# Optimization experiments

Measured on AMD Instinct MI355X. Metric: run time of the kernel, lower is better.

The kernel has to match this reference:

```python
import jax, jax.numpy as jnp
import numpy as np

H = 1024   # hidden_size
I = 2048   # intermediate_size
E = 16     # num_experts
K = 2      # num_experts_per_tok
B, T = 2, 2048


def setup_inputs() -> dict:
    key = jax.random.key(0)
    k1, k2, k3, k4 = jax.random.split(key, 4)
    x = jax.random.normal(k1, (B, T, H), dtype=jnp.float32)
    # torch nn.Linear weight layout: [out_features, in_features]
    Wg = jax.random.normal(k2, (E, H), dtype=jnp.float32) * 0.02   # gate
    W1 = jax.random.normal(k3, (E, I, H), dtype=jnp.float32) * 0.02  # fc1 per expert
    W2 = jax.random.normal(k4, (E, H, I), dtype=jnp.float32) * 0.02  # fc2 per expert
    return {"x": x, "Wg": Wg, "W1": W1, "W2": W2}


def reference(x, Wg, W1, W2):
    Bq, Tq, Hq = x.shape
    nt = Bq * Tq
    x_flat = x.reshape(nt, Hq)                       # [nt, H]
    gate_logits = x_flat @ Wg.T                      # [nt, E]
    gate_probs = jax.nn.softmax(gate_logits, axis=-1)
    topk_vals, topk_idx = jax.lax.top_k(gate_probs, K)  # [nt, K]
    # dense combine weights: zero for unselected (token, expert) pairs
    rows = jnp.arange(nt)[:, None]                   # [nt, 1]
    cw = jnp.zeros((nt, E), dtype=x.dtype).at[rows, topk_idx].add(topk_vals)
    # per-expert dense SiLU-MLP; combine weight of 0 makes unselected
    # contributions exactly zero, matching the original gather/scatter math.
    y_flat = jnp.zeros_like(x_flat)
    for e in range(E):
        h = jax.nn.silu(x_flat @ W1[e].T)            # [nt, I]
        o = h @ W2[e].T                              # [nt, H]
        y_flat = y_flat + cw[:, e:e + 1] * o
    return y_flat.reshape(Bq, Tq, Hq)
```

## Files before the change

kernel.cpp:

```cpp
#include <hip/hip_runtime.h>
#include <hip/hip_bf16.h>

#define H_DIM 1024
#define I_DIM 2048
#define NEXP  16
#define NTOK  4096
#define BM 128
#define BN 128
#define BK 32
#define ABUF (BM*BK)
#define BBUF (BN*BK)
#define MAXS 10240
#define MAXRB (MAXS/BM)
#define PAIRS (NTOK*2)
#define SORT_T 256
#define PPT (PAIRS/SORT_T)

typedef __attribute__((ext_vector_type(8))) short short8;
typedef __attribute__((ext_vector_type(4))) short short4v;
typedef __attribute__((ext_vector_type(4))) float f32x4;

#define OFF_TOKE 256
#define OFF_TOKW (OFF_TOKE + PAIRS*4)
#define OFF_TOS  (OFF_TOKW + PAIRS*4)
#define OFF_WOS  (OFF_TOS + MAXS*4)
#define OFF_H    (OFF_WOS + MAXS*4)
#define OFF_XBF  (OFF_H + (size_t)MAXS*I_DIM*2)
#define OFF_WBF  (OFF_XBF + (size_t)NTOK*H_DIM*2)
#define NEED_FULL (OFF_WBF + (size_t)NEXP*I_DIM*H_DIM*2)

#define GLDS16(gsrc, ldst) \
  __builtin_amdgcn_global_load_lds((const __attribute__((address_space(1))) void*)(gsrc), \
                                   (__attribute__((address_space(3))) void*)(ldst), 16, 0, 0)

__device__ inline short f2bf(float f) {
    union { float f; unsigned u; } v; v.f = f;
    unsigned u = v.u + 0x7FFFu + ((v.u >> 16) & 1u);
    return (short)(u >> 16);
}

__device__ inline short8 pack8(const float4 a, const float4 b) {
    return (short8){ f2bf(a.x), f2bf(a.y), f2bf(a.z), f2bf(a.w),
                     f2bf(b.x), f2bf(b.y), f2bf(b.z), f2bf(b.w) };
}

__global__ __launch_bounds__(256) void conv_kernel(
    const float* __restrict__ src, short* __restrict__ dst, int n8)
{
    int i = blockIdx.x * blockDim.x + threadIdx.x;
    const int stride = gridDim.x * blockDim.x;
    for (; i < n8; i += stride) {
        const float4 f0 = ((const float4*)src)[2*i];
        const float4 f1 = ((const float4*)src)[2*i+1];
        ((short8*)dst)[i] = pack8(f0, f1);
    }
}

template<bool WRITE_XBF>
__global__ __launch_bounds__(256) void gate_kernel(
    const float* __restrict__ x, const float* __restrict__ Wg,
    int* __restrict__ tokE, float* __restrict__ tokW, short* __restrict__ xbf)
{
    const int tok  = blockIdx.x * 4 + (threadIdx.x >> 6);
    const int lane = threadIdx.x & 63;
    const float4* xr = (const float4*)(x + (size_t)tok * H_DIM);

    float acc[NEXP];
#pragma unroll
    for (int e = 0; e < NEXP; e++) acc[e] = 0.f;
#pragma unroll
    for (int j = 0; j < H_DIM/4; j += 64) {
        const float4 xv = xr[j + lane];
        if constexpr (WRITE_XBF) {
            *(short4v*)(xbf + (size_t)tok * H_DIM + (j + lane) * 4) =
                (short4v){ f2bf(xv.x), f2bf(xv.y), f2bf(xv.z), f2bf(xv.w) };
        }
#pragma unroll
        for (int e = 0; e < NEXP; e++) {
            const float4 wv = ((const float4*)(Wg + e * H_DIM))[j + lane];
            acc[e] = fmaf(xv.x, wv.x, fmaf(xv.y, wv.y, fmaf(xv.z, wv.z, fmaf(xv.w, wv.w, acc[e]))));
        }
    }
#pragma unroll
    for (int off = 32; off; off >>= 1) {
#pragma unroll
        for (int e = 0; e < NEXP; e++) acc[e] += __shfl_xor(acc[e], off, 64);
    }
    if (lane == 0) {
        float m = acc[0];
#pragma unroll
        for (int e = 1; e < NEXP; e++) m = fmaxf(m, acc[e]);
        float p[NEXP]; float s = 0.f;
#pragma unroll
        for (int e = 0; e < NEXP; e++) { p[e] = __expf(acc[e] - m); s += p[e]; }
        int i1 = 0;
#pragma unroll
        for (int e = 1; e < NEXP; e++) if (acc[e] > acc[i1]) i1 = e;
        int i2 = -1;
#pragma unroll
        for (int e = 0; e < NEXP; e++) {
            if (e == i1) continue;
            if (i2 < 0 || acc[e] > acc[i2]) i2 = e;
        }
        const float inv = 1.f / s;
        tokE[tok*2+0] = i1; tokW[tok*2+0] = p[i1] * inv;
        tokE[tok*2+1] = i2; tokW[tok*2+1] = p[i2] * inv;
    }
}

__global__ __launch_bounds__(SORT_T) void sort_kernel(
    const int* __restrict__ tokE, const float* __restrict__ tokW,
    int* __restrict__ aoff, int* __restrict__ tok_of_slot, float* __restrict__ w_of_slot)
{
    __shared__ int hist[NEXP * SORT_T];
    __shared__ int tot[NEXP];
    __shared__ int aoff_l[NEXP + 1];

    const int tid = threadIdx.x;
    const int lane = tid & 63, wv = tid >> 6;

    int eloc[PPT];
#pragma unroll
    for (int i = 0; i < PPT; i++) eloc[i] = tokE[tid * PPT + i];

#pragma unroll
    for (int e = 0; e < NEXP; e++) hist[e * SORT_T + tid] = 0;
    __syncthreads();
#pragma unroll
    for (int i = 0; i < PPT; i++) hist[eloc[i] * SORT_T + tid]++;
    __syncthreads();

#pragma unroll
    for (int r = 0; r < 4; r++) {
        const int e = wv * 4 + r;
        const int base = e * SORT_T + lane * 4;
        int v0 = hist[base+0], v1 = hist[base+1], v2 = hist[base+2], v3 = hist[base+3];
        const int s = v0 + v1 + v2 + v3;
        int incl = s;
#pragma unroll
        for (int off = 1; off < 64; off <<= 1) {
            const int t = __shfl_up(incl, off, 64);
            if (lane >= off) incl += t;
        }
        int run = incl - s;
        hist[base+0] = run; run += v0;
        hist[base+1] = run; run += v1;
        hist[base+2] = run; run += v2;
        hist[base+3] = run;
        if (lane == 63) tot[e] = incl;
    }
    __syncthreads();

    if (tid == 0) {
        int acc = 0;
#pragma unroll
        for (int e = 0; e < NEXP; e++) {
            aoff_l[e] = acc; aoff[e] = acc;
            acc += ((tot[e] + BM - 1) / BM) * BM;
        }
        aoff_l[NEXP] = acc; aoff[NEXP] = acc;
    }
    __syncthreads();

#pragma unroll
    for (int i = 0; i < PPT; i++) {
        const int p = tid * PPT + i;
        const int e = eloc[i];
        const int idx = hist[e * SORT_T + tid]++;
        const int slot = aoff_l[e] + idx;
        tok_of_slot[slot] = p >> 1;
        w_of_slot[slot] = tokW[p];
    }
}

template<int MODE>
__global__ __launch_bounds__(256) void fc1_kernel_t(
    const void* __restrict__ xsrc, const void* __restrict__ w1src,
    const int* __restrict__ aoff, const int* __restrict__ tok_of_slot,
    short* __restrict__ h)
{
    const int total = aoff[NEXP];
    const int row0 = blockIdx.y * BM;
    if (row0 >= total) return;
    int e = 0;
    while (aoff[e+1] <= row0) e++;
    const int col0 = blockIdx.x * BN;

    __shared__ short As[2*ABUF];
    __shared__ short Bs[2*BBUF];

    const int tid = threadIdx.x, wid = tid>>6, lane = tid&63;
    const int wr = wid>>1, wc = wid&1;

    const int srow = wid*32 + (lane>>2);
    const int skc  = (lane&3)*8;

    int t0 = tok_of_slot[row0 + srow];      if (t0 < 0) t0 = 0;
    int t1 = tok_of_slot[row0 + srow + 16]; if (t1 < 0) t1 = 0;

    const short *sa0=nullptr,*sa1=nullptr,*sb0=nullptr,*sb1=nullptr;
    const float *fa0=nullptr,*fa1=nullptr,*fb0=nullptr,*fb1=nullptr;
    if constexpr (MODE == 0) {
        const short* xb = (const short*)xsrc;
        const short* wb = (const short*)w1src + (size_t)e * I_DIM * H_DIM;
        sa0 = xb + (size_t)t0 * H_DIM + skc;
        sa1 = xb + (size_t)t1 * H_DIM + skc;
        sb0 = wb + (size_t)(col0 + srow)      * H_DIM + skc;
        sb1 = wb + (size_t)(col0 + srow + 16) * H_DIM + skc;
    } else {
        const float* xf = (const float*)xsrc;
        const float* wf = (const float*)w1src + (size_t)e * I_DIM * H_DIM;
        fa0 = xf + (size_t)t0 * H_DIM + skc;
        fa1 = xf + (size_t)t1 * H_DIM + skc;
        fb0 = wf + (size_t)(col0 + srow)      * H_DIM + skc;
        fb1 = wf + (size_t)(col0 + srow + 16) * H_DIM + skc;
    }
    short* la0 = &As[(wid*2+0)*512];
    short* la1 = &As[(wid*2+1)*512];
    short* lb0 = &Bs[(wid*2+0)*512];
    short* lb1 = &Bs[(wid*2+1)*512];

    const int frow = lane & 15, fko = (lane>>4)*8;

    f32x4 acc[4][4];
#pragma unroll
    for (int m=0;m<4;m++)
#pragma unroll
        for (int n=0;n<4;n++) acc[m][n] = (f32x4){0.f,0.f,0.f,0.f};

#define FC1_STAGE(buf, k)                                                     \
    if constexpr (MODE == 0) {                                                \
        GLDS16(sa0 + (k), la0 + (buf)*ABUF);                                  \
        GLDS16(sa1 + (k), la1 + (buf)*ABUF);                                  \
        GLDS16(sb0 + (k), lb0 + (buf)*BBUF);                                  \
        GLDS16(sb1 + (k), lb1 + (buf)*BBUF);                                  \
    } else {                                                                  \
        const float4 a00 = *(const float4*)(fa0+(k)), a01 = *(const float4*)(fa0+(k)+4); \
        const float4 a10 = *(const float4*)(fa1+(k)), a11 = *(const float4*)(fa1+(k)+4); \
        const float4 b00 = *(const float4*)(fb0+(k)), b01 = *(const float4*)(fb0+(k)+4); \
        const float4 b10 = *(const float4*)(fb1+(k)), b11 = *(const float4*)(fb1+(k)+4); \
        *(short8*)&As[(buf)*ABUF + srow*32 + skc]      = pack8(a00, a01);     \
        *(short8*)&As[(buf)*ABUF + (srow+16)*32 + skc] = pack8(a10, a11);     \
        *(short8*)&Bs[(buf)*BBUF + srow*32 + skc]      = pack8(b00, b01);     \
        *(short8*)&Bs[(buf)*BBUF + (srow+16)*32 + skc] = pack8(b10, b11);     \
    }

    FC1_STAGE(0, 0);
    __syncthreads();

    const int NT = H_DIM / BK;
    int cur = 0;
    for (int t = 0; t < NT; ++t) {
        if (t + 1 < NT) { FC1_STAGE(cur ^ 1, (t + 1) * BK); }

        short8 af[4], bfr[4];
#pragma unroll
        for (int m=0;m<4;m++) af[m]  = *(const short8*)&As[cur*ABUF + (wr*64 + m*16 + frow)*32 + fko];
#pragma unroll
        for (int n=0;n<4;n++) bfr[n] = *(const short8*)&Bs[cur*BBUF + (wc*64 + n*16 + frow)*32 + fko];
#pragma unroll
        for (int m=0;m<4;m++)
#pragma unroll
            for (int n=0;n<4;n++)
                acc[m][n] = __builtin_amdgcn_mfma_f32_16x16x32_bf16(af[m], bfr[n], acc[m][n], 0, 0, 0);

        __syncthreads();
        cur ^= 1;
    }
#undef FC1_STAGE

    const int mr0 = row0 + wr*64 + (lane>>4)*4;
    const int nc0 = col0 + wc*64 + (lane&15);
#pragma unroll
    for (int m=0;m<4;m++)
#pragma unroll
        for (int n=0;n<4;n++)
#pragma unroll
            for (int r=0;r<4;r++) {
                const float v = acc[m][n][r];
                const float sv = v / (1.f + __expf(-v));
                h[(size_t)(mr0 + m*16 + r) * I_DIM + nc0 + n*16] = f2bf(sv);
            }
}

template<int MODE>
__global__ __launch_bounds__(256) void fc2_kernel_t(
    const short* __restrict__ h, const void* __restrict__ w2src,
    const int* __restrict__ aoff, const int* __restrict__ tok_of_slot,
    const float* __restrict__ w_of_slot, float* __restrict__ y)
{
    const int total = aoff[NEXP];
    const int row0 = blockIdx.y * BM;
    if (row0 >= total) return;
    int e = 0;
    while (aoff[e+1] <= row0) e++;
    const int col0 = blockIdx.x * BN;

    __shared__ short As[2*ABUF];
    __shared__ short Bs[2*BBUF];

    const int tid = threadIdx.x, wid = tid>>6, lane = tid&63;
    const int wr = wid>>1, wc = wid&1;

    const int srow = wid*32 + (lane>>2);
    const int skc  = (lane&3)*8;

    const short* sa0 = h + (size_t)(row0 + srow)      * I_DIM + skc;
    const short* sa1 = h + (size_t)(row0 + srow + 16) * I_DIM + skc;

    const short *sb0=nullptr,*sb1=nullptr;
    const float *fb0=nullptr,*fb1=nullptr;
    if constexpr (MODE == 0) {
        const short* wb = (const short*)w2src + (size_t)e * H_DIM * I_DIM;
        sb0 = wb + (size_t)(col0 + srow)      * I_DIM + skc;
        sb1 = wb + (size_t)(col0 + srow + 16) * I_DIM + skc;
    } else {
        const float* wf = (const float*)w2src + (size_t)e * H_DIM * I_DIM;
        fb0 = wf + (size_t)(col0 + srow)      * I_DIM + skc;
        fb1 = wf + (size_t)(col0 + srow + 16) * I_DIM + skc;
    }
    short* la0 = &As[(wid*2+0)*512];
    short* la1 = &As[(wid*2+1)*512];
    short* lb0 = &Bs[(wid*2+0)*512];
    short* lb1 = &Bs[(wid*2+1)*512];

    const int frow = lane & 15, fko = (lane>>4)*8;

    f32x4 acc[4][4];
#pragma unroll
    for (int m=0;m<4;m++)
#pragma unroll
        for (int n=0;n<4;n++) acc[m][n] = (f32x4){0.f,0.f,0.f,0.f};

#define FC2_STAGE(buf, k)                                                     \
    {                                                                         \
        GLDS16(sa0 + (k), la0 + (buf)*ABUF);                                  \
        GLDS16(sa1 + (k), la1 + (buf)*ABUF);                                  \
        if constexpr (MODE == 0) {                                            \
            GLDS16(sb0 + (k), lb0 + (buf)*BBUF);                              \
            GLDS16(sb1 + (k), lb1 + (buf)*BBUF);                              \
        } else {                                                              \
            const float4 b00 = *(const float4*)(fb0+(k)), b01 = *(const float4*)(fb0+(k)+4); \
            const float4 b10 = *(const float4*)(fb1+(k)), b11 = *(const float4*)(fb1+(k)+4); \
            *(short8*)&Bs[(buf)*BBUF + srow*32 + skc]      = pack8(b00, b01); \
            *(short8*)&Bs[(buf)*BBUF + (srow+16)*32 + skc] = pack8(b10, b11); \
        }                                                                     \
    }

    FC2_STAGE(0, 0);
    __syncthreads();

    const int NT = I_DIM / BK;
    int cur = 0;
    for (int t = 0; t < NT; ++t) {
        if (t + 1 < NT) { FC2_STAGE(cur ^ 1, (t + 1) * BK); }

        short8 af[4], bfr[4];
#pragma unroll
        for (int m=0;m<4;m++) af[m]  = *(const short8*)&As[cur*ABUF + (wr*64 + m*16 + frow)*32 + fko];
#pragma unroll
        for (int n=0;n<4;n++) bfr[n] = *(const short8*)&Bs[cur*BBUF + (wc*64 + n*16 + frow)*32 + fko];
#pragma unroll
        for (int m=0;m<4;m++)
#pragma unroll
            for (int n=0;n<4;n++)
                acc[m][n] = __builtin_amdgcn_mfma_f32_16x16x32_bf16(af[m], bfr[n], acc[m][n], 0, 0, 0);

        __syncthreads();
        cur ^= 1;
    }
#undef FC2_STAGE

    const int mr0 = row0 + wr*64 + (lane>>4)*4;
    const int nc0 = col0 + wc*64 + (lane&15);
#pragma unroll
    for (int m=0;m<4;m++)
#pragma unroll
        for (int r=0;r<4;r++) {
            const int slot = mr0 + m*16 + r;
            const int tok = tok_of_slot[slot];
            if (tok < 0) continue;
            const float w = w_of_slot[slot];
#pragma unroll
            for (int n=0;n<4;n++)
                atomicAdd(&y[(size_t)tok * H_DIM + nc0 + n*16], w * acc[m][n][r]);
        }
}

extern "C" void kernel_launch(void* const* d_in, const int* in_sizes, int n_in,
                              void* d_out, int out_size, void* d_ws, size_t ws_size,
                              hipStream_t stream) {
    const float* x  = (const float*)d_in[0];
    const float* Wg = (const float*)d_in[1];
    const float* W1 = (const float*)d_in[2];
    const float* W2 = (const float*)d_in[3];
    float* y = (float*)d_out;

    char* ws = (char*)d_ws;
    int*   aoff        = (int*)  (ws + 128);
    int*   tokE        = (int*)  (ws + OFF_TOKE);
    float* tokW        = (float*)(ws + OFF_TOKW);
    int*   tok_of_slot = (int*)  (ws + OFF_TOS);
    float* w_of_slot   = (float*)(ws + OFF_WOS);
    short* h           = (short*)(ws + OFF_H);
    short* xbf         = (short*)(ws + OFF_XBF);
    short* wbf         = (short*)(ws + OFF_WBF);

    const bool full = (ws_size >= NEED_FULL);

    hipMemsetAsync(tok_of_slot, 0xFF, MAXS*4, stream);
    hipMemsetAsync(y, 0, (size_t)out_size * 4, stream);

    if (full) {
        gate_kernel<true><<<NTOK/4, 256, 0, stream>>>(x, Wg, tokE, tokW, xbf);
        sort_kernel<<<1, SORT_T, 0, stream>>>(tokE, tokW, aoff, tok_of_slot, w_of_slot);
        conv_kernel<<<2048, 256, 0, stream>>>(W1, wbf, NEXP*I_DIM*H_DIM/8);
        fc1_kernel_t<0><<<dim3(I_DIM/BN, MAXRB), 256, 0, stream>>>(xbf, wbf, aoff, tok_of_slot, h);
        conv_kernel<<<2048, 256, 0, stream>>>(W2, wbf, NEXP*H_DIM*I_DIM/8);
        fc2_kernel_t<0><<<dim3(H_DIM/BN, MAXRB), 256, 0, stream>>>(h, wbf, aoff, tok_of_slot, w_of_slot, y);
    } else {
        gate_kernel<false><<<NTOK/4, 256, 0, stream>>>(x, Wg, tokE, tokW, nullptr);
        sort_kernel<<<1, SORT_T, 0, stream>>>(tokE, tokW, aoff, tok_of_slot, w_of_slot);
        fc1_kernel_t<1><<<dim3(I_DIM/BN, MAXRB), 256, 0, stream>>>(x, W1, aoff, tok_of_slot, h);
        fc2_kernel_t<1><<<dim3(H_DIM/BN, MAXRB), 256, 0, stream>>>(h, W2, aoff, tok_of_slot, w_of_slot, y);
    }
}
```

Before: 278.0 us.

## Convert fp32 expert weights to bf16 inside GEMM loads, drop pre-conversion passes

Removes the two standalone kernels that converted all of W1 and W2 to bf16 in workspace. The fc1/fc2 kernels now read fp32 weights directly into registers, issue those loads before the MFMA block and write them to LDS as bf16 afterwards, so load latency is hidden behind compute. It also flattens the grid to 1D with an XCD-aware block swizzle to improve L2 locality. This avoids writing and re-reading about 128MB of converted weights, at the cost of doubled weight bytes per tile read and extra VALU packing inside the main loop.

```diff
diff --git a/kernel.cpp b/kernel.cpp
--- a/kernel.cpp
+++ b/kernel.cpp
@@ -12,6 +12,8 @@
 #define BBUF (BN*BK)
 #define MAXS 10240
 #define MAXRB (MAXS/BM)
+#define NC1 (I_DIM/BN)
+#define NC2 (H_DIM/BN)
 #define PAIRS (NTOK*2)
 #define SORT_T 256
 #define PPT (PAIRS/SORT_T)
@@ -26,8 +28,7 @@
 #define OFF_WOS  (OFF_TOS + MAXS*4)
 #define OFF_H    (OFF_WOS + MAXS*4)
 #define OFF_XBF  (OFF_H + (size_t)MAXS*I_DIM*2)
-#define OFF_WBF  (OFF_XBF + (size_t)NTOK*H_DIM*2)
-#define NEED_FULL (OFF_WBF + (size_t)NEXP*I_DIM*H_DIM*2)
+#define NEED_XBF (OFF_XBF + (size_t)NTOK*H_DIM*2)
 
 #define GLDS16(gsrc, ldst) \
   __builtin_amdgcn_global_load_lds((const __attribute__((address_space(1))) void*)(gsrc), \
@@ -44,16 +45,8 @@
                      f2bf(b.x), f2bf(b.y), f2bf(b.z), f2bf(b.w) };
 }
 
-__global__ __launch_bounds__(256) void conv_kernel(
-    const float* __restrict__ src, short* __restrict__ dst, int n8)
-{
-    int i = blockIdx.x * blockDim.x + threadIdx.x;
-    const int stride = gridDim.x * blockDim.x;
-    for (; i < n8; i += stride) {
-        const float4 f0 = ((const float4*)src)[2*i];
-        const float4 f1 = ((const float4*)src)[2*i+1];
-        ((short8*)dst)[i] = pack8(f0, f1);
-    }
+__device__ inline int xcd_swz(int bid, int nwg) {
+    return (bid & 7) * (nwg >> 3) + (bid >> 3);
 }
 
 template<bool WRITE_XBF>
@@ -173,52 +166,48 @@
     }
 }
 
-template<int MODE>
+template<int AMODE>
 __global__ __launch_bounds__(256) void fc1_kernel_t(
-    const void* __restrict__ xsrc, const void* __restrict__ w1src,
+    const void* __restrict__ xsrc, const float* __restrict__ W1,
     const int* __restrict__ aoff, const int* __restrict__ tok_of_slot,
     short* __restrict__ h)
 {
+    const int wg = xcd_swz(blockIdx.x, NC1 * MAXRB);
+    const int colb = wg % NC1, rowb = wg / NC1;
     const int total = aoff[NEXP];
-    const int row0 = blockIdx.y * BM;
+    const int row0 = rowb * BM;
     if (row0 >= total) return;
     int e = 0;
     while (aoff[e+1] <= row0) e++;
-    const int col0 = blockIdx.x * BN;
+    const int col0 = colb * BN;
 
     __shared__ short As[2*ABUF];
     __shared__ short Bs[2*BBUF];
 
     const int tid = threadIdx.x, wid = tid>>6, lane = tid&63;
     const int wr = wid>>1, wc = wid&1;
-
     const int srow = wid*32 + (lane>>2);
     const int skc  = (lane&3)*8;
 
     int t0 = tok_of_slot[row0 + srow];      if (t0 < 0) t0 = 0;
     int t1 = tok_of_slot[row0 + srow + 16]; if (t1 < 0) t1 = 0;
 
-    const short *sa0=nullptr,*sa1=nullptr,*sb0=nullptr,*sb1=nullptr;
-    const float *fa0=nullptr,*fa1=nullptr,*fb0=nullptr,*fb1=nullptr;
-    if constexpr (MODE == 0) {
+    const float* wf0 = W1 + (size_t)e * I_DIM * H_DIM + (size_t)(col0 + srow)      * H_DIM + skc;
+    const float* wf1 = W1 + (size_t)e * I_DIM * H_DIM + (size_t)(col0 + srow + 16) * H_DIM + skc;
+
+    const short *sa0=nullptr,*sa1=nullptr;
+    const float *fa0=nullptr,*fa1=nullptr;
+    if constexpr (AMODE == 0) {
         const short* xb = (const short*)xsrc;
-        const short* wb = (const short*)w1src + (size_t)e * I_DIM * H_DIM;
         sa0 = xb + (size_t)t0 * H_DIM + skc;
         sa1 = xb + (size_t)t1 * H_DIM + skc;
-        sb0 = wb + (size_t)(col0 + srow)      * H_DIM + skc;
-        sb1 = wb + (size_t)(col0 + srow + 16) * H_DIM + skc;
     } else {
         const float* xf = (const float*)xsrc;
-        const float* wf = (const float*)w1src + (size_t)e * I_DIM * H_DIM;
         fa0 = xf + (size_t)t0 * H_DIM + skc;
         fa1 = xf + (size_t)t1 * H_DIM + skc;
-        fb0 = wf + (size_t)(col0 + srow)      * H_DIM + skc;
-        fb1 = wf + (size_t)(col0 + srow + 16) * H_DIM + skc;
     }
     short* la0 = &As[(wid*2+0)*512];
     short* la1 = &As[(wid*2+1)*512];
-    short* lb0 = &Bs[(wid*2+0)*512];
-    short* lb1 = &Bs[(wid*2+1)*512];
 
     const int frow = lane & 15, fko = (lane>>4)*8;
 
@@ -228,30 +217,38 @@
 #pragma unroll
         for (int n=0;n<4;n++) acc[m][n] = (f32x4){0.f,0.f,0.f,0.f};
 
-#define FC1_STAGE(buf, k)                                                     \
-    if constexpr (MODE == 0) {                                                \
-        GLDS16(sa0 + (k), la0 + (buf)*ABUF);                                  \
-        GLDS16(sa1 + (k), la1 + (buf)*ABUF);                                  \
-        GLDS16(sb0 + (k), lb0 + (buf)*BBUF);                                  \
-        GLDS16(sb1 + (k), lb1 + (buf)*BBUF);                                  \
-    } else {                                                                  \
-        const float4 a00 = *(const float4*)(fa0+(k)), a01 = *(const float4*)(fa0+(k)+4); \
-        const float4 a10 = *(const float4*)(fa1+(k)), a11 = *(const float4*)(fa1+(k)+4); \
-        const float4 b00 = *(const float4*)(fb0+(k)), b01 = *(const float4*)(fb0+(k)+4); \
-        const float4 b10 = *(const float4*)(fb1+(k)), b11 = *(const float4*)(fb1+(k)+4); \
-        *(short8*)&As[(buf)*ABUF + srow*32 + skc]      = pack8(a00, a01);     \
-        *(short8*)&As[(buf)*ABUF + (srow+16)*32 + skc] = pack8(a10, a11);     \
-        *(short8*)&Bs[(buf)*BBUF + srow*32 + skc]      = pack8(b00, b01);     \
-        *(short8*)&Bs[(buf)*BBUF + (srow+16)*32 + skc] = pack8(b10, b11);     \
-    }
-
-    FC1_STAGE(0, 0);
+    float4 b00 = *(const float4*)(wf0), b01 = *(const float4*)(wf0+4);
+    float4 b10 = *(const float4*)(wf1), b11 = *(const float4*)(wf1+4);
+    float4 a00, a01, a10, a11;
+    if constexpr (AMODE == 0) {
+        GLDS16(sa0, la0);
+        GLDS16(sa1, la1);
+    } else {
+        a00 = *(const float4*)(fa0); a01 = *(const float4*)(fa0+4);
+        a10 = *(const float4*)(fa1); a11 = *(const float4*)(fa1+4);
+        *(short8*)&As[srow*32 + skc]      = pack8(a00, a01);
+        *(short8*)&As[(srow+16)*32 + skc] = pack8(a10, a11);
+    }
+    *(short8*)&Bs[srow*32 + skc]      = pack8(b00, b01);
+    *(short8*)&Bs[(srow+16)*32 + skc] = pack8(b10, b11);
     __syncthreads();
 
     const int NT = H_DIM / BK;
     int cur = 0;
     for (int t = 0; t < NT; ++t) {
-        if (t + 1 < NT) { FC1_STAGE(cur ^ 1, (t + 1) * BK); }
+        const int kn = (t+1)*BK;
+        const bool more = (t+1 < NT);
+        if (more) {
+            if constexpr (AMODE == 0) {
+                GLDS16(sa0 + kn, la0 + (cur^1)*ABUF);
+                GLDS16(sa1 + kn, la1 + (cur^1)*ABUF);
+            } else {
+                a00 = *(const float4*)(fa0+kn); a01 = *(const float4*)(fa0+kn+4);
+                a10 = *(const float4*)(fa1+kn); a11 = *(const float4*)(fa1+kn+4);
+            }
+            b00 = *(const float4*)(wf0+kn); b01 = *(const float4*)(wf0+kn+4);
+            b10 = *(const float4*)(wf1+kn); b11 = *(const float4*)(wf1+kn+4);
+        }
 
         short8 af[4], bfr[4];
 #pragma unroll
@@ -264,10 +261,17 @@
             for (int n=0;n<4;n++)
                 acc[m][n] = __builtin_amdgcn_mfma_f32_16x16x32_bf16(af[m], bfr[n], acc[m][n], 0, 0, 0);
 
+        if (more) {
+            if constexpr (AMODE == 1) {
+                *(short8*)&As[(cur^1)*ABUF + srow*32 + skc]      = pack8(a00, a01);
+                *(short8*)&As[(cur^1)*ABUF + (srow+16)*32 + skc] = pack8(a10, a11);
+            }
+            *(short8*)&Bs[(cur^1)*BBUF + srow*32 + skc]      = pack8(b00, b01);
+            *(short8*)&Bs[(cur^1)*BBUF + (srow+16)*32 + skc] = pack8(b10, b11);
+        }
         __syncthreads();
         cur ^= 1;
     }
-#undef FC1_STAGE
 
     const int mr0 = row0 + wr*64 + (lane>>4)*4;
     const int nc0 = col0 + wc*64 + (lane&15);
@@ -283,46 +287,36 @@
             }
 }
 
-template<int MODE>
-__global__ __launch_bounds__(256) void fc2_kernel_t(
-    const short* __restrict__ h, const void* __restrict__ w2src,
+__global__ __launch_bounds__(256) void fc2_kernel(
+    const short* __restrict__ h, const float* __restrict__ W2,
     const int* __restrict__ aoff, const int* __restrict__ tok_of_slot,
     const float* __restrict__ w_of_slot, float* __restrict__ y)
 {
+    const int wg = xcd_swz(blockIdx.x, NC2 * MAXRB);
+    const int colb = wg % NC2, rowb = wg / NC2;
     const int total = aoff[NEXP];
-    const int row0 = blockIdx.y * BM;
+    const int row0 = rowb * BM;
     if (row0 >= total) return;
     int e = 0;
     while (aoff[e+1] <= row0) e++;
-    const int col0 = blockIdx.x * BN;
+    const int col0 = colb * BN;
 
     __shared__ short As[2*ABUF];
     __shared__ short Bs[2*BBUF];
 
     const int tid = threadIdx.x, wid = tid>>6, lane = tid&63;
     const int wr = wid>>1, wc = wid&1;
-
     const int srow = wid*32 + (lane>>2);
     const int skc  = (lane&3)*8;
 
     const short* sa0 = h + (size_t)(row0 + srow)      * I_DIM + skc;
     const short* sa1 = h + (size_t)(row0 + srow + 16) * I_DIM + skc;
 
-    const short *sb0=nullptr,*sb1=nullptr;
-    const float *fb0=nullptr,*fb1=nullptr;
-    if constexpr (MODE == 0) {
-        const short* wb = (const short*)w2src + (size_t)e * H_DIM * I_DIM;
-        sb0 = wb + (size_t)(col0 + srow)      * I_DIM + skc;
-        sb1 = wb + (size_t)(col0 + srow + 16) * I_DIM + skc;
-    } else {
-        const float* wf = (const float*)w2src + (size_t)e * H_DIM * I_DIM;
-        fb0 = wf + (size_t)(col0 + srow)      * I_DIM + skc;
-        fb1 = wf + (size_t)(col0 + srow + 16) * I_DIM + skc;
-    }
+    const float* wf0 = W2 + (size_t)e * H_DIM * I_DIM + (size_t)(col0 + srow)      * I_DIM + skc;
+    const float* wf1 = W2 + (size_t)e * H_DIM * I_DIM + (size_t)(col0 + srow + 16) * I_DIM + skc;
+
     short* la0 = &As[(wid*2+0)*512];
     short* la1 = &As[(wid*2+1)*512];
-    short* lb0 = &Bs[(wid*2+0)*512];
-    short* lb1 = &Bs[(wid*2+1)*512];
 
     const int frow = lane & 15, fko = (lane>>4)*8;
 
@@ -332,28 +326,25 @@
 #pragma unroll
         for (int n=0;n<4;n++) acc[m][n] = (f32x4){0.f,0.f,0.f,0.f};
 
-#define FC2_STAGE(buf, k)                                                     \
-    {                                                                         \
-        GLDS16(sa0 + (k), la0 + (buf)*ABUF);                                  \
-        GLDS16(sa1 + (k), la1 + (buf)*ABUF);                                  \
-        if constexpr (MODE == 0) {                                            \
-            GLDS16(sb0 + (k), lb0 + (buf)*BBUF);                              \
-            GLDS16(sb1 + (k), lb1 + (buf)*BBUF);                              \
-        } else {                                                              \
-            const float4 b00 = *(const float4*)(fb0+(k)), b01 = *(const float4*)(fb0+(k)+4); \
-            const float4 b10 = *(const float4*)(fb1+(k)), b11 = *(const float4*)(fb1+(k)+4); \
-            *(short8*)&Bs[(buf)*BBUF + srow*32 + skc]      = pack8(b00, b01); \
-            *(short8*)&Bs[(buf)*BBUF + (srow+16)*32 + skc] = pack8(b10, b11); \
-        }                                                                     \
-    }
-
-    FC2_STAGE(0, 0);
+    float4 b00 = *(const float4*)(wf0), b01 = *(const float4*)(wf0+4);
+    float4 b10 = *(const float4*)(wf1), b11 = *(const float4*)(wf1+4);
+    GLDS16(sa0, la0);
+    GLDS16(sa1, la1);
+    *(short8*)&Bs[srow*32 + skc]      = pack8(b00, b01);
+    *(short8*)&Bs[(srow+16)*32 + skc] = pack8(b10, b11);
     __syncthreads();
 
     const int NT = I_DIM / BK;
     int cur = 0;
     for (int t = 0; t < NT; ++t) {
-        if (t + 1 < NT) { FC2_STAGE(cur ^ 1, (t + 1) * BK); }
+        const int kn = (t+1)*BK;
+        const bool more = (t+1 < NT);
+        if (more) {
+            GLDS16(sa0 + kn, la0 + (cur^1)*ABUF);
+            GLDS16(sa1 + kn, la1 + (cur^1)*ABUF);
+            b00 = *(const float4*)(wf0+kn); b01 = *(const float4*)(wf0+kn+4);
+            b10 = *(const float4*)(wf1+kn); b11 = *(const float4*)(wf1+kn+4);
+        }
 
         short8 af[4], bfr[4];
 #pragma unroll
@@ -366,10 +357,13 @@
             for (int n=0;n<4;n++)
                 acc[m][n] = __builtin_amdgcn_mfma_f32_16x16x32_bf16(af[m], bfr[n], acc[m][n], 0, 0, 0);
 
+        if (more) {
+            *(short8*)&Bs[(cur^1)*BBUF + srow*32 + skc]      = pack8(b00, b01);
+            *(short8*)&Bs[(cur^1)*BBUF + (srow+16)*32 + skc] = pack8(b10, b11);
+        }
         __syncthreads();
         cur ^= 1;
     }
-#undef FC2_STAGE
 
     const int mr0 = row0 + wr*64 + (lane>>4)*4;
     const int nc0 = col0 + wc*64 + (lane&15);
@@ -404,24 +398,20 @@
     float* w_of_slot   = (float*)(ws + OFF_WOS);
     short* h           = (short*)(ws + OFF_H);
     short* xbf         = (short*)(ws + OFF_XBF);
-    short* wbf         = (short*)(ws + OFF_WBF);
-
-    const bool full = (ws_size >= NEED_FULL);
+
+    const bool hasXbf = (ws_size >= NEED_XBF);
 
     hipMemsetAsync(tok_of_slot, 0xFF, MAXS*4, stream);
     hipMemsetAsync(y, 0, (size_t)out_size * 4, stream);
 
-    if (full) {
+    if (hasXbf) {
         gate_kernel<true><<<NTOK/4, 256, 0, stream>>>(x, Wg, tokE, tokW, xbf);
         sort_kernel<<<1, SORT_T, 0, stream>>>(tokE, tokW, aoff, tok_of_slot, w_of_slot);
-        conv_kernel<<<2048, 256, 0, stream>>>(W1, wbf, NEXP*I_DIM*H_DIM/8);
-        fc1_kernel_t<0><<<dim3(I_DIM/BN, MAXRB), 256, 0, stream>>>(xbf, wbf, aoff, tok_of_slot, h);
-        conv_kernel<<<2048, 256, 0, stream>>>(W2, wbf, NEXP*H_DIM*I_DIM/8);
-        fc2_kernel_t<0><<<dim3(H_DIM/BN, MAXRB), 256, 0, stream>>>(h, wbf, aoff, tok_of_slot, w_of_slot, y);
+        fc1_kernel_t<0><<<NC1*MAXRB, 256, 0, stream>>>(xbf, W1, aoff, tok_of_slot, h);
     } else {
         gate_kernel<false><<<NTOK/4, 256, 0, stream>>>(x, Wg, tokE, tokW, nullptr);
         sort_kernel<<<1, SORT_T, 0, stream>>>(tokE, tokW, aoff, tok_of_slot, w_of_slot);
-        fc1_kernel_t<1><<<dim3(I_DIM/BN, MAXRB), 256, 0, stream>>>(x, W1, aoff, tok_of_slot, h);
-        fc2_kernel_t<1><<<dim3(H_DIM/BN, MAXRB), 256, 0, stream>>>(h, W2, aoff, tok_of_slot, w_of_slot, y);
-    }
-}
+        fc1_kernel_t<1><<<NC1*MAXRB, 256, 0, stream>>>(x, W1, aoff, tok_of_slot, h);
+    }
+    fc2_kernel<<<NC2*MAXRB, 256, 0, stream>>>(h, W2, aoff, tok_of_slot, w_of_slot, y);
+}
```

New measurement: 261.8 us (median of 2 runs). 1.06x faster.
